# Optimization experiments

Measured on AMD Instinct MI355X. Metric: run time of the kernel, lower is better.

Reference implementation:

```python
import jax, jax.numpy as jnp
import numpy as np

DIM = 2048
N_HEADS = 16
N_KV_HEADS = 4
HEAD_DIM = DIM // N_HEADS  # 128
N_REP = N_HEADS // N_KV_HEADS
EPS = 1e-6


def rmsnorm(x, w):
    norm = jax.lax.rsqrt(jnp.mean(x * x, axis=-1, keepdims=True) + EPS)
    return x * norm * w


def apply_rope(xq, xk, freqs_cis):
    # xq: (B,S,Hq,D), xk: (B,S,Hk,D); freqs_cis: (S, D/2, 2) -> (cos, sin)
    cos = freqs_cis[None, :, None, :, 0]  # (1,S,1,D/2)
    sin = freqs_cis[None, :, None, :, 1]

    def rot(x):
        xr = x.reshape(*x.shape[:-1], HEAD_DIM // 2, 2)
        x0, x1 = xr[..., 0], xr[..., 1]
        o0 = x0 * cos - x1 * sin
        o1 = x0 * sin + x1 * cos
        return jnp.stack([o0, o1], axis=-1).reshape(x.shape)

    return rot(xq), rot(xk)


def setup_inputs() -> dict:
    key = jax.random.key(0)
    k1, k2, k3, k4, k5, k6 = jax.random.split(key, 6)
    B, S = 2, 2048
    x = jax.random.normal(k1, (B, S, DIM), dtype=jnp.float32)
    x_mask = jnp.ones((B, S), dtype=bool)
    freqs_cis = jax.random.uniform(k2, (S, HEAD_DIM // 2, 2), dtype=jnp.float32)
    qkv_out = (N_HEADS + 2 * N_KV_HEADS) * HEAD_DIM  # 3072
    w_qkv = jax.random.normal(k3, (qkv_out, DIM), dtype=jnp.float32) * (DIM ** -0.5)
    w_out = jax.random.normal(k4, (DIM, N_HEADS * HEAD_DIM), dtype=jnp.float32) * (DIM ** -0.5)
    qn_w = jnp.ones((HEAD_DIM,), dtype=jnp.float32)
    kn_w = jnp.ones((HEAD_DIM,), dtype=jnp.float32)
    return {"x": x, "x_mask": x_mask, "freqs_cis": freqs_cis,
            "w_qkv": w_qkv, "w_out": w_out, "qn_w": qn_w, "kn_w": kn_w}


def reference(x, x_mask, freqs_cis, w_qkv, w_out, qn_w, kn_w):
    B, S, _ = x.shape
    qkv = x @ w_qkv.T  # (B,S,3072)
    dq = N_HEADS * HEAD_DIM
    dkv = N_KV_HEADS * HEAD_DIM
    xq = qkv[..., :dq].reshape(B, S, N_HEADS, HEAD_DIM)
    xk = qkv[..., dq:dq + dkv].reshape(B, S, N_KV_HEADS, HEAD_DIM)
    xv = qkv[..., dq + dkv:].reshape(B, S, N_KV_HEADS, HEAD_DIM)
    xq = rmsnorm(xq, qn_w)
    xk = rmsnorm(xk, kn_w)
    xq, xk = apply_rope(xq, xk, freqs_cis)
    # GQA: repeat kv heads
    xk = jnp.repeat(xk, N_REP, axis=2)  # (B,S,H,D)
    xv = jnp.repeat(xv, N_REP, axis=2)
    # SDPA: (B,H,S,D)
    q = jnp.moveaxis(xq, 1, 2)
    k = jnp.moveaxis(xk, 1, 2)
    v = jnp.moveaxis(xv, 1, 2)
    scale = HEAD_DIM ** -0.5
    scores = jnp.einsum('bhqd,bhkd->bhqk', q, k) * scale
    bias = jnp.where(x_mask[:, None, None, :], 0.0, -jnp.inf).astype(q.dtype)
    attn = jax.nn.softmax(scores + bias, axis=-1)
    out = jnp.einsum('bhqk,bhkd->bhqd', attn, v)
    out = jnp.moveaxis(out, 1, 2).reshape(B, S, N_HEADS * HEAD_DIM)
    return out @ w_out.T
```

## Files before the change

### kernel.cpp

```cpp
#include <hip/hip_runtime.h>
#include <hip/hip_bf16.h>

#define DIMSZ 2048
#define SLEN  2048
#define NH    16
#define NKV   4
#define HD    128
#define NTOK  4096
#define QKVN  3072

typedef __bf16 bf16x8 __attribute__((ext_vector_type(8)));
typedef __bf16 bf16x4 __attribute__((ext_vector_type(4)));
typedef short  s16x4  __attribute__((ext_vector_type(4)));
typedef float  floatx4 __attribute__((ext_vector_type(4)));

__device__ __forceinline__ void async16(const __bf16* g, __bf16* l) {
    __builtin_amdgcn_global_load_lds(
        (const __attribute__((address_space(1))) void*)g,
        (__attribute__((address_space(3))) void*)l, 16, 0, 0);
}

__device__ __forceinline__ floatx4 mfma16x16x16_bf16(s16x4 a, s16x4 b, floatx4 c) {
#if __has_builtin(__builtin_amdgcn_mfma_f32_16x16x16bf16_1k)
    return __builtin_amdgcn_mfma_f32_16x16x16bf16_1k(a, b, c, 0, 0, 0);
#else
    asm volatile("v_mfma_f32_16x16x16_bf16 %0, %1, %2, %0"
                 : "+v"(c) : "v"(a), "v"(b));
    return c;
#endif
}

__global__ __launch_bounds__(256) void cvt3(const float* __restrict__ s0, __bf16* __restrict__ d0, int n0,
                                            const float* __restrict__ s1, __bf16* __restrict__ d1, int n1,
                                            const float* __restrict__ s2, __bf16* __restrict__ d2, int n2) {
    int blk = blockIdx.x;
    int b0 = n0 >> 11, b1 = n1 >> 11;
    const float* s; __bf16* d; int base;
    if (blk < b0)           { s = s0; d = d0; base = blk << 11; }
    else if (blk < b0 + b1) { s = s1; d = d1; base = (blk - b0) << 11; }
    else                    { s = s2; d = d2; base = (blk - b0 - b1) << 11; }
    int i = base + threadIdx.x * 8;
    float4 a = *(const float4*)(s + i);
    float4 b = *(const float4*)(s + i + 4);
    bf16x8 o;
    o[0] = (__bf16)a.x; o[1] = (__bf16)a.y; o[2] = (__bf16)a.z; o[3] = (__bf16)a.w;
    o[4] = (__bf16)b.x; o[5] = (__bf16)b.y; o[6] = (__bf16)b.z; o[7] = (__bf16)b.w;
    *(bf16x8*)(d + i) = o;
}

template <typename CT>
__global__ __launch_bounds__(256) void gemm_bt(const __bf16* __restrict__ A,
                                               const __bf16* __restrict__ B,
                                               CT* __restrict__ C,
                                               int M, int N, int K) {
    __shared__ __align__(16) __bf16 As[2][128 * 64];
    __shared__ __align__(16) __bf16 Bs[2][128 * 64];
    const int tid  = threadIdx.x;
    const int wave = tid >> 6, lane = tid & 63;
    const int lr = lane & 15, lq = lane >> 4;
    const int wm = (wave >> 1) * 64, wn = (wave & 1) * 64;
    const int tm0 = blockIdx.y * 128, tn0 = blockIdx.x * 128;

    floatx4 acc[4][4] = {};

    auto stage = [&](int buf, int k0) {
#pragma unroll
        for (int i = 0; i < 4; ++i) {
            int c   = tid + 256 * i;
            int row = c >> 3, col = (c & 7) * 8;
            async16(&A[(size_t)(tm0 + row) * K + k0 + col], &As[buf][c * 8]);
            async16(&B[(size_t)(tn0 + row) * K + k0 + col], &Bs[buf][c * 8]);
        }
    };

    const int nIter = K >> 6;
    stage(0, 0);
    for (int it = 0; it < nIter; ++it) {
        const int buf = it & 1;
        __syncthreads();
        if (it + 1 < nIter) stage(buf ^ 1, (it + 1) << 6);
#pragma unroll
        for (int kk = 0; kk < 2; ++kk) {
            bf16x8 af[4], bg[4];
#pragma unroll
            for (int i = 0; i < 4; ++i)
                af[i] = *(const bf16x8*)&As[buf][(wm + i * 16 + lr) * 64 + kk * 32 + lq * 8];
#pragma unroll
            for (int j = 0; j < 4; ++j)
                bg[j] = *(const bf16x8*)&Bs[buf][(wn + j * 16 + lr) * 64 + kk * 32 + lq * 8];
#pragma unroll
            for (int i = 0; i < 4; ++i)
#pragma unroll
                for (int j = 0; j < 4; ++j)
                    acc[i][j] = __builtin_amdgcn_mfma_f32_16x16x32_bf16(
                        af[i], bg[j], acc[i][j], 0, 0, 0);
        }
    }
#pragma unroll
    for (int i = 0; i < 4; ++i)
#pragma unroll
        for (int j = 0; j < 4; ++j)
#pragma unroll
            for (int r = 0; r < 4; ++r) {
                int row = tm0 + wm + i * 16 + lq * 4 + r;
                int col = tn0 + wn + j * 16 + lr;
                C[(size_t)row * N + col] = (CT)acc[i][j][r];
            }
}

__global__ __launch_bounds__(256) void prep(const __bf16* __restrict__ qkv,
                                            const float* __restrict__ freqs,
                                            const float* __restrict__ qn_w,
                                            const float* __restrict__ kn_w,
                                            __bf16* __restrict__ Qo,
                                            __bf16* __restrict__ Ko,
                                            __bf16* __restrict__ VT) {
    if (blockIdx.y < 20) {
        const int tok = blockIdx.x * 4 + (threadIdx.x >> 6);
        const int hd  = blockIdx.y;
        const int t   = threadIdx.x & 63;
        const int s   = tok & (SLEN - 1);
        const int b   = tok >> 11;
        const bool isq = hd < NH;
        const int h    = isq ? hd : hd - NH;
        const int base = isq ? h * HD : (NH * HD + h * HD);

        const __bf16* src = qkv + (size_t)tok * QKVN + base + 2 * t;
        float x0 = (float)src[0], x1 = (float)src[1];
        float ss = x0 * x0 + x1 * x1;
#pragma unroll
        for (int off = 32; off >= 1; off >>= 1) ss += __shfl_xor(ss, off);
        float rs = rsqrtf(ss * (1.0f / 128.0f) + 1e-6f);

        const float* w = isq ? qn_w : kn_w;
        float w0 = w[2 * t], w1 = w[2 * t + 1];
        float cs = freqs[(s * 64 + t) * 2 + 0];
        float sn = freqs[(s * 64 + t) * 2 + 1];
        float n0 = x0 * rs * w0, n1 = x1 * rs * w1;
        float o0 = n0 * cs - n1 * sn;
        float o1 = n0 * sn + n1 * cs;
        if (isq) { o0 *= 0.08838834764831845f; o1 *= 0.08838834764831845f; }

        __bf16* dst = isq ? (Qo + (((size_t)(b * NH + h)) * SLEN + s) * HD + 2 * t)
                          : (Ko + (((size_t)(b * NKV + h)) * SLEN + s) * HD + 2 * t);
        dst[0] = (__bf16)o0;
        dst[1] = (__bf16)o1;
    } else {
        if (blockIdx.x >= 256) return;
        __shared__ __align__(16) __bf16 L[64 * 136];
        const int kh  = blockIdx.x >> 6;
        const int b   = (blockIdx.x >> 5) & 1;
        const int st  = blockIdx.x & 31;
        const int tid = threadIdx.x;
#pragma unroll
        for (int i = 0; i < 4; ++i) {
            int c = tid + 256 * i;
            int srow = c >> 4, dc = (c & 15) * 8;
            int tok = b * SLEN + st * 64 + srow;
            *(int4*)&L[srow * 136 + dc] =
                *(const int4*)&qkv[(size_t)tok * QKVN + 2560 + kh * HD + dc];
        }
        __syncthreads();
#pragma unroll
        for (int i = 0; i < 4; ++i) {
            int c = tid + 256 * i;
            int d = c >> 3, sc = (c & 7) * 8;
            __bf16 tmp[8];
#pragma unroll
            for (int j = 0; j < 8; ++j) tmp[j] = L[(sc + j) * 136 + d];
            *(int4*)&VT[(((size_t)(b * NKV + kh)) * HD + d) * SLEN + st * 64 + sc] =
                *(int4*)tmp;
        }
    }
}

__global__ __launch_bounds__(256) void attn(const __bf16* __restrict__ Q,
                                            const __bf16* __restrict__ Kn,
                                            const __bf16* __restrict__ VT,
                                            __bf16* __restrict__ O) {
    __shared__ __align__(16) __bf16 Ks [2][64 * 128];
    __shared__ __align__(16) __bf16 Vts[2][128 * 64];
    const int qt  = blockIdx.x;
    const int h   = blockIdx.y;
    const int b   = blockIdx.z;
    const int tid = threadIdx.x;
    const int w = tid >> 6, lane = tid & 63, lr = lane & 15, lq = lane >> 4;
    const int kh = h >> 2;

    const __bf16* Qb = Q  + ((size_t)(b * NH + h))   * SLEN * HD;
    const __bf16* Kb = Kn + ((size_t)(b * NKV + kh)) * SLEN * HD;
    const __bf16* Vb = VT + ((size_t)(b * NKV + kh)) * HD * SLEN;

    bf16x8 qf[2][4];
    const int qbase = qt * 128 + w * 32;
#pragma unroll
    for (int g2 = 0; g2 < 2; ++g2)
#pragma unroll
        for (int kc = 0; kc < 4; ++kc)
            qf[g2][kc] = *(const bf16x8*)
                &Qb[(size_t)(qbase + g2 * 16 + lr) * HD + kc * 32 + lq * 8];

    floatx4 oacc[2][8] = {};
    float l_i[2] = {0.f, 0.f};

    auto stage = [&](int buf, int kt) {
#pragma unroll
        for (int i = 0; i < 4; ++i) {
            int c = tid + 256 * i;
            int row = c >> 4, u = c & 15;
            int g = u ^ (row & 7);
            async16(&Kb[(size_t)(kt * 64 + row) * HD + g * 8], &Ks[buf][c * 8]);
        }
#pragma unroll
        for (int i = 0; i < 4; ++i) {
            int c = tid + 256 * i;
            int d = c >> 3, u = c & 7;
            int g = u ^ (d & 7);
            async16(&Vb[(size_t)d * SLEN + kt * 64 + g * 8], &Vts[buf][c * 8]);
        }
    };

    stage(0, 0);
    for (int kt = 0; kt < 32; ++kt) {
        const int buf = kt & 1;
        __syncthreads();
        if (kt < 31) stage(buf ^ 1, kt + 1);

        floatx4 sacc[2][4] = {};
#pragma unroll
        for (int nt = 0; nt < 4; ++nt)
#pragma unroll
            for (int kc = 0; kc < 4; ++kc) {
                bf16x8 kf = *(const bf16x8*)
                    &Ks[buf][(nt * 16 + lr) * 128 + ((kc * 4 + lq) ^ (lr & 7)) * 8];
                sacc[0][nt] = __builtin_amdgcn_mfma_f32_16x16x32_bf16(
                    kf, qf[0][kc], sacc[0][nt], 0, 0, 0);
                sacc[1][nt] = __builtin_amdgcn_mfma_f32_16x16x32_bf16(
                    kf, qf[1][kc], sacc[1][nt], 0, 0, 0);
            }

        s16x4 pf[2][4];
#pragma unroll
        for (int g2 = 0; g2 < 2; ++g2) {
            float rsum = 0.f;
#pragma unroll
            for (int nt = 0; nt < 4; ++nt) {
                bf16x4 pb;
#pragma unroll
                for (int r = 0; r < 4; ++r) {
                    float p = __expf(sacc[g2][nt][r]);
                    rsum += p;
                    pb[r] = (__bf16)p;
                }
                pf[g2][nt] = *(s16x4*)&pb;
            }
            l_i[g2] += rsum;
        }

#pragma unroll
        for (int dt = 0; dt < 8; ++dt)
#pragma unroll
            for (int nt = 0; nt < 4; ++nt) {
                int u = (2 * nt + (lq >> 1)) ^ (lr & 7);
                s16x4 vf = *(const s16x4*)
                    &Vts[buf][(dt * 16 + lr) * 64 + u * 8 + (lq & 1) * 4];
                oacc[0][dt] = mfma16x16x16_bf16(vf, pf[0][nt], oacc[0][dt]);
                oacc[1][dt] = mfma16x16x16_bf16(vf, pf[1][nt], oacc[1][dt]);
            }
    }

#pragma unroll
    for (int g2 = 0; g2 < 2; ++g2) {
        float l = l_i[g2];
        l += __shfl_xor(l, 16);
        l += __shfl_xor(l, 32);
        float inv = 1.0f / l;
        int qs = qbase + g2 * 16 + lr;
        __bf16* orow = O + (((size_t)(b * SLEN + qs)) * NH + h) * HD;
#pragma unroll
        for (int dt = 0; dt < 8; ++dt) {
            bf16x4 ob;
#pragma unroll
            for (int r = 0; r < 4; ++r) ob[r] = (__bf16)(oacc[g2][dt][r] * inv);
            *(bf16x4*)&orow[dt * 16 + lq * 4] = ob;
        }
    }
}

extern "C" void kernel_launch(void* const* d_in, const int* in_sizes, int n_in,
                              void* d_out, int out_size, void* d_ws, size_t ws_size,
                              hipStream_t stream) {
    const float* x     = (const float*)d_in[0];
    const float* freqs = (const float*)d_in[2];
    const float* w_qkv = (const float*)d_in[3];
    const float* w_out = (const float*)d_in[4];
    const float* qn_w  = (const float*)d_in[5];
    const float* kn_w  = (const float*)d_in[6];
    float* out = (float*)d_out;

    char* ws = (char*)d_ws;
    __bf16* qkv = (__bf16*)ws;
    __bf16* Qb  = (__bf16*)(ws + 25165824ull);
    __bf16* Kb  = (__bf16*)(ws + 25165824ull + 16777216);
    __bf16* VTb = (__bf16*)(ws + 25165824ull + 16777216 + 4194304);
    __bf16* xb  = (__bf16*)(ws + 50331648ull);
    __bf16* wqb = (__bf16*)(ws + 50331648ull + 16777216);
    __bf16* wob = (__bf16*)(ws + 50331648ull + 16777216 + 12582912);
    __bf16* Ob  = (__bf16*)ws;

    cvt3<<<dim3((NTOK * DIMSZ + QKVN * DIMSZ + DIMSZ * DIMSZ) / 2048), 256, 0, stream>>>(
        x, xb, NTOK * DIMSZ, w_qkv, wqb, QKVN * DIMSZ, w_out, wob, DIMSZ * DIMSZ);

    gemm_bt<__bf16><<<dim3(QKVN / 128, NTOK / 128), 256, 0, stream>>>(
        xb, wqb, qkv, NTOK, QKVN, DIMSZ);

    prep<<<dim3(NTOK / 4, 21), 256, 0, stream>>>(qkv, freqs, qn_w, kn_w, Qb, Kb, VTb);

    attn<<<dim3(SLEN / 128, NH, 2), 256, 0, stream>>>(Qb, Kb, VTb, Ob);

    gemm_bt<float><<<dim3(DIMSZ / 128, NTOK / 128), 256, 0, stream>>>(
        Ob, wob, out, NTOK, DIMSZ, DIMSZ);
}
```

Before: 357.5 us.

## Switch attention to 32x32x16 MFMA with split-K waves and LDS reduction

The attention kernel now uses 32x32x16 bf16 MFMA tiles instead of 16x16 tiles. Each pair of waves splits the 64-key tile in half, and each wave covers 64 queries. The P matrix is rearranged with cross-half lane shuffles so it can feed the PV MFMA. Partial outputs and row sums are combined through LDS at the end. The aim is fewer MFMA issues and fewer LDS fragment reads per FLOP, at the cost of shuffles, a final reduction and a larger shared-memory footprint, with launch bounds now requesting two blocks.

```diff
diff --git a/kernel.cpp b/kernel.cpp
--- a/kernel.cpp
+++ b/kernel.cpp
@@ -11,23 +11,14 @@
 
 typedef __bf16 bf16x8 __attribute__((ext_vector_type(8)));
 typedef __bf16 bf16x4 __attribute__((ext_vector_type(4)));
-typedef short  s16x4  __attribute__((ext_vector_type(4)));
-typedef float  floatx4 __attribute__((ext_vector_type(4)));
+typedef __bf16 bf16x2 __attribute__((ext_vector_type(2)));
+typedef float  floatx4  __attribute__((ext_vector_type(4)));
+typedef float  floatx16 __attribute__((ext_vector_type(16)));
 
 __device__ __forceinline__ void async16(const __bf16* g, __bf16* l) {
     __builtin_amdgcn_global_load_lds(
         (const __attribute__((address_space(1))) void*)g,
         (__attribute__((address_space(3))) void*)l, 16, 0, 0);
-}
-
-__device__ __forceinline__ floatx4 mfma16x16x16_bf16(s16x4 a, s16x4 b, floatx4 c) {
-#if __has_builtin(__builtin_amdgcn_mfma_f32_16x16x16bf16_1k)
-    return __builtin_amdgcn_mfma_f32_16x16x16bf16_1k(a, b, c, 0, 0, 0);
-#else
-    asm volatile("v_mfma_f32_16x16x16_bf16 %0, %1, %2, %0"
-                 : "+v"(c) : "v"(a), "v"(b));
-    return c;
-#endif
 }
 
 __global__ __launch_bounds__(256) void cvt3(const float* __restrict__ s0, __bf16* __restrict__ d0, int n0,
@@ -174,33 +165,39 @@
     }
 }
 
-__global__ __launch_bounds__(256) void attn(const __bf16* __restrict__ Q,
-                                            const __bf16* __restrict__ Kn,
-                                            const __bf16* __restrict__ VT,
-                                            __bf16* __restrict__ O) {
-    __shared__ __align__(16) __bf16 Ks [2][64 * 128];
-    __shared__ __align__(16) __bf16 Vts[2][128 * 64];
+__global__ __launch_bounds__(256, 2) void attn(const __bf16* __restrict__ Q,
+                                               const __bf16* __restrict__ Kn,
+                                               const __bf16* __restrict__ VT,
+                                               __bf16* __restrict__ O) {
+    __shared__ __align__(16) char smem[66048];
+    __bf16* KsB  = (__bf16*)smem;
+    __bf16* VtsB = (__bf16*)(smem + 32768);
+    float*  lpool = (float*)(smem + 65536);
+    float*  opool = (float*)smem;
+
     const int qt  = blockIdx.x;
-    const int h   = blockIdx.y;
+    const int hh  = blockIdx.y;
     const int b   = blockIdx.z;
     const int tid = threadIdx.x;
-    const int w = tid >> 6, lane = tid & 63, lr = lane & 15, lq = lane >> 4;
-    const int kh = h >> 2;
-
-    const __bf16* Qb = Q  + ((size_t)(b * NH + h))   * SLEN * HD;
+    const int w = tid >> 6, lane = tid & 63, l31 = lane & 31;
+    const bool hi = lane >= 32;
+    const int qset = w >> 1, khalf = w & 1;
+    const int kh = hh >> 2;
+
+    const __bf16* Qb = Q  + ((size_t)(b * NH + hh))  * SLEN * HD;
     const __bf16* Kb = Kn + ((size_t)(b * NKV + kh)) * SLEN * HD;
     const __bf16* Vb = VT + ((size_t)(b * NKV + kh)) * HD * SLEN;
 
-    bf16x8 qf[2][4];
-    const int qbase = qt * 128 + w * 32;
-#pragma unroll
-    for (int g2 = 0; g2 < 2; ++g2)
-#pragma unroll
-        for (int kc = 0; kc < 4; ++kc)
-            qf[g2][kc] = *(const bf16x8*)
-                &Qb[(size_t)(qbase + g2 * 16 + lr) * HD + kc * 32 + lq * 8];
-
-    floatx4 oacc[2][8] = {};
+    bf16x8 qf[2][8];
+    const int qbase = qt * 128 + qset * 64;
+#pragma unroll
+    for (int qg = 0; qg < 2; ++qg)
+#pragma unroll
+        for (int kc = 0; kc < 8; ++kc)
+            qf[qg][kc] = *(const bf16x8*)
+                &Qb[(size_t)(qbase + qg * 32 + l31) * HD + kc * 16 + (hi ? 8 : 0)];
+
+    floatx16 oacc[2][4] = {};
     float l_i[2] = {0.f, 0.f};
 
     auto stage = [&](int buf, int kt) {
@@ -209,14 +206,14 @@
             int c = tid + 256 * i;
             int row = c >> 4, u = c & 15;
             int g = u ^ (row & 7);
-            async16(&Kb[(size_t)(kt * 64 + row) * HD + g * 8], &Ks[buf][c * 8]);
+            async16(&Kb[(size_t)(kt * 64 + row) * HD + g * 8], &KsB[buf * 8192 + c * 8]);
         }
 #pragma unroll
         for (int i = 0; i < 4; ++i) {
             int c = tid + 256 * i;
             int d = c >> 3, u = c & 7;
             int g = u ^ (d & 7);
-            async16(&Vb[(size_t)d * SLEN + kt * 64 + g * 8], &Vts[buf][c * 8]);
+            async16(&Vb[(size_t)d * SLEN + kt * 64 + g * 8], &VtsB[buf * 8192 + c * 8]);
         }
     };
 
@@ -225,64 +222,104 @@
         const int buf = kt & 1;
         __syncthreads();
         if (kt < 31) stage(buf ^ 1, kt + 1);
-
-        floatx4 sacc[2][4] = {};
-#pragma unroll
-        for (int nt = 0; nt < 4; ++nt)
-#pragma unroll
-            for (int kc = 0; kc < 4; ++kc) {
-                bf16x8 kf = *(const bf16x8*)
-                    &Ks[buf][(nt * 16 + lr) * 128 + ((kc * 4 + lq) ^ (lr & 7)) * 8];
-                sacc[0][nt] = __builtin_amdgcn_mfma_f32_16x16x32_bf16(
-                    kf, qf[0][kc], sacc[0][nt], 0, 0, 0);
-                sacc[1][nt] = __builtin_amdgcn_mfma_f32_16x16x32_bf16(
-                    kf, qf[1][kc], sacc[1][nt], 0, 0, 0);
+        const __bf16* Ksb  = KsB  + buf * 8192;
+        const __bf16* Vtsb = VtsB + buf * 8192;
+
+        floatx16 s0 = {}, s1 = {};
+#pragma unroll
+        for (int kc = 0; kc < 8; ++kc) {
+            bf16x8 kf = *(const bf16x8*)
+                &Ksb[(khalf * 32 + l31) * 128 + (((kc * 2 + (hi ? 1 : 0)) ^ (l31 & 7)) * 8)];
+            s0 = __builtin_amdgcn_mfma_f32_32x32x16_bf16(kf, qf[0][kc], s0, 0, 0, 0);
+            s1 = __builtin_amdgcn_mfma_f32_32x32x16_bf16(kf, qf[1][kc], s1, 0, 0, 0);
+        }
+
+        int pv0[8], pv1[8];
+        float r0 = 0.f, r1 = 0.f;
+#pragma unroll
+        for (int i = 0; i < 8; ++i) {
+            float e0 = __expf(s0[2 * i]), e1 = __expf(s0[2 * i + 1]);
+            r0 += e0 + e1;
+            bf16x2 t0 = {(__bf16)e0, (__bf16)e1};
+            pv0[i] = *(int*)&t0;
+            float f0 = __expf(s1[2 * i]), f1 = __expf(s1[2 * i + 1]);
+            r1 += f0 + f1;
+            bf16x2 t1 = {(__bf16)f0, (__bf16)f1};
+            pv1[i] = *(int*)&t1;
+        }
+        l_i[0] += r0; l_i[1] += r1;
+
+        int bf0[2][4], bf1[2][4];
+#pragma unroll
+        for (int kd = 0; kd < 2; ++kd) {
+            int base = 4 * kd;
+            int a2 = __shfl_xor(pv0[base + 2], 32), a3 = __shfl_xor(pv0[base + 3], 32);
+            int a0 = __shfl_xor(pv0[base + 0], 32), a1 = __shfl_xor(pv0[base + 1], 32);
+            bf0[kd][0] = hi ? a2 : pv0[base + 0];
+            bf0[kd][1] = hi ? a3 : pv0[base + 1];
+            bf0[kd][2] = hi ? pv0[base + 2] : a0;
+            bf0[kd][3] = hi ? pv0[base + 3] : a1;
+            int c2 = __shfl_xor(pv1[base + 2], 32), c3 = __shfl_xor(pv1[base + 3], 32);
+            int c0 = __shfl_xor(pv1[base + 0], 32), c1 = __shfl_xor(pv1[base + 1], 32);
+            bf1[kd][0] = hi ? c2 : pv1[base + 0];
+            bf1[kd][1] = hi ? c3 : pv1[base + 1];
+            bf1[kd][2] = hi ? pv1[base + 2] : c0;
+            bf1[kd][3] = hi ? pv1[base + 3] : c1;
+        }
+
+#pragma unroll
+        for (int dt = 0; dt < 4; ++dt) {
+            int drow = dt * 32 + l31;
+#pragma unroll
+            for (int kd = 0; kd < 2; ++kd) {
+                bf16x8 vf = *(const bf16x8*)
+                    &Vtsb[drow * 64 + (((khalf * 4 + kd * 2 + (hi ? 1 : 0)) ^ (l31 & 7)) * 8)];
+                oacc[0][dt] = __builtin_amdgcn_mfma_f32_32x32x16_bf16(
+                    vf, *(bf16x8*)&bf0[kd][0], oacc[0][dt], 0, 0, 0);
+                oacc[1][dt] = __builtin_amdgcn_mfma_f32_32x32x16_bf16(
+                    vf, *(bf16x8*)&bf1[kd][0], oacc[1][dt], 0, 0, 0);
             }
-
-        s16x4 pf[2][4];
-#pragma unroll
-        for (int g2 = 0; g2 < 2; ++g2) {
-            float rsum = 0.f;
-#pragma unroll
-            for (int nt = 0; nt < 4; ++nt) {
-                bf16x4 pb;
-#pragma unroll
-                for (int r = 0; r < 4; ++r) {
-                    float p = __expf(sacc[g2][nt][r]);
-                    rsum += p;
-                    pb[r] = (__bf16)p;
+        }
+    }
+
+    l_i[0] += __shfl_xor(l_i[0], 32);
+    l_i[1] += __shfl_xor(l_i[1], 32);
+    __syncthreads();
+    if (khalf == 1) {
+#pragma unroll
+        for (int qg = 0; qg < 2; ++qg)
+#pragma unroll
+            for (int dt = 0; dt < 4; ++dt)
+#pragma unroll
+                for (int rq = 0; rq < 4; ++rq) {
+                    float4 v = {oacc[qg][dt][rq * 4 + 0], oacc[qg][dt][rq * 4 + 1],
+                                oacc[qg][dt][rq * 4 + 2], oacc[qg][dt][rq * 4 + 3]};
+                    *(float4*)&opool[qset * 8192 + (qg * 4 + dt) * 1024 + rq * 256 + lane * 4] = v;
                 }
-                pf[g2][nt] = *(s16x4*)&pb;
-            }
-            l_i[g2] += rsum;
-        }
-
-#pragma unroll
-        for (int dt = 0; dt < 8; ++dt)
-#pragma unroll
-            for (int nt = 0; nt < 4; ++nt) {
-                int u = (2 * nt + (lq >> 1)) ^ (lr & 7);
-                s16x4 vf = *(const s16x4*)
-                    &Vts[buf][(dt * 16 + lr) * 64 + u * 8 + (lq & 1) * 4];
-                oacc[0][dt] = mfma16x16x16_bf16(vf, pf[0][nt], oacc[0][dt]);
-                oacc[1][dt] = mfma16x16x16_bf16(vf, pf[1][nt], oacc[1][dt]);
-            }
-    }
-
-#pragma unroll
-    for (int g2 = 0; g2 < 2; ++g2) {
-        float l = l_i[g2];
-        l += __shfl_xor(l, 16);
-        l += __shfl_xor(l, 32);
-        float inv = 1.0f / l;
-        int qs = qbase + g2 * 16 + lr;
-        __bf16* orow = O + (((size_t)(b * SLEN + qs)) * NH + h) * HD;
-#pragma unroll
-        for (int dt = 0; dt < 8; ++dt) {
-            bf16x4 ob;
-#pragma unroll
-            for (int r = 0; r < 4; ++r) ob[r] = (__bf16)(oacc[g2][dt][r] * inv);
-            *(bf16x4*)&orow[dt * 16 + lq * 4] = ob;
+        if (!hi) {
+            lpool[qset * 64 + l31]      = l_i[0];
+            lpool[qset * 64 + 32 + l31] = l_i[1];
+        }
+    }
+    __syncthreads();
+    if (khalf == 0) {
+#pragma unroll
+        for (int qg = 0; qg < 2; ++qg) {
+            float inv = 1.0f / (l_i[qg] + lpool[qset * 64 + qg * 32 + l31]);
+            int s = qbase + qg * 32 + l31;
+            __bf16* orow = O + (((size_t)(b * SLEN + s)) * NH + hh) * HD;
+#pragma unroll
+            for (int dt = 0; dt < 4; ++dt)
+#pragma unroll
+                for (int rq = 0; rq < 4; ++rq) {
+                    float4 p = *(float4*)&opool[qset * 8192 + (qg * 4 + dt) * 1024 + rq * 256 + lane * 4];
+                    bf16x4 ob;
+                    ob[0] = (__bf16)((oacc[qg][dt][rq * 4 + 0] + p.x) * inv);
+                    ob[1] = (__bf16)((oacc[qg][dt][rq * 4 + 1] + p.y) * inv);
+                    ob[2] = (__bf16)((oacc[qg][dt][rq * 4 + 2] + p.z) * inv);
+                    ob[3] = (__bf16)((oacc[qg][dt][rq * 4 + 3] + p.w) * inv);
+                    *(bf16x4*)&orow[dt * 32 + rq * 8 + (hi ? 4 : 0)] = ob;
+                }
         }
     }
 }
```

Result: slower. 375.0 us (+4.9%).
